# Kernel tuning notes

Hardware: AMD Instinct MI355X
Metric: run time of the kernel (lower is better)

## Reference

```python
import jax, jax.numpy as jnp
import numpy as np

N = 262144
D = 128  # hidden_dim
NUM_RULES = 5


def setup_inputs() -> dict:
    key = jax.random.key(0)
    ks = jax.random.split(key, 7)
    h_fused = jax.random.normal(ks[0], (N, D), dtype=jnp.float32)
    entity_types = jax.random.randint(ks[1], (N,), 0, 3)
    entity_masks = jnp.ones((N,), dtype=bool)
    # rule_scorer params (torch nn.Linear convention: y = x @ W.T + b)
    W1 = jax.random.normal(ks[2], (D, 3 * D), dtype=jnp.float32) * (1.0 / np.sqrt(3 * D))
    b1 = jnp.zeros((D,), dtype=jnp.float32)
    W2 = jax.random.normal(ks[3], (1, D), dtype=jnp.float32) * (1.0 / np.sqrt(D))
    b2 = jnp.zeros((1,), dtype=jnp.float32)
    rule_table = jax.random.normal(ks[4], (NUM_RULES, D), dtype=jnp.float32) * 0.1
    return {"h_fused": h_fused, "entity_types": entity_types,
            "entity_masks": entity_masks, "rule_id": 0,
            "W1": W1, "b1": b1, "W2": W2, "b2": b2, "rule_table": rule_table}


def reference(h_fused, entity_types, entity_masks, rule_id, W1, b1, W2, b2, rule_table):
    # masks per entity type
    car_mask = (entity_types == 0) & entity_masks
    light_mask = (entity_types == 1) & entity_masks
    stop_mask = (entity_types == 2) & entity_masks

    def masked_mean(mask):
        mf = mask.astype(h_fused.dtype)[:, None]            # [N,1]
        cnt = mf.sum()
        s = (h_fused * mf).sum(axis=0)                      # [D]
        return jnp.where(cnt > 0, s / jnp.maximum(cnt, 1.0), 0.0)

    h_light = masked_mean(light_mask)  # [D] - pooled once (original redundantly recomputes per car)
    h_stop = masked_mean(stop_mask)    # [D]

    n = h_fused.shape[0]
    concat = jnp.concatenate([
        h_fused,
        jnp.broadcast_to(h_light, (n, D)),
        jnp.broadcast_to(h_stop, (n, D)),
    ], axis=1)                                              # [N, 3D]

    hid = jax.nn.relu(concat @ W1.T + b1)                   # [N, D] (dropout = identity, eval)
    beta = jax.nn.sigmoid(hid @ W2.T + b2)[:, 0]            # [N]

    rule_emb = rule_table[rule_id]                          # [D]
    h_car = beta[:, None] * h_fused + (1.0 - beta[:, None]) * rule_emb
    h_out = jnp.where(car_mask[:, None], h_car, h_fused)    # [N, D]
    beta_out = jnp.where(car_mask, beta, 0.0)               # [N]; original compacts to [N_car]
    return h_out, beta_out
```

## Files before the change

kernel.cpp:

```cpp
#include <hip/hip_runtime.h>
#include <hip/hip_bf16.h>

#define D 128

typedef __attribute__((ext_vector_type(8))) short short8;
typedef __attribute__((ext_vector_type(4))) float f32x4;

__device__ __forceinline__ unsigned short f2bf(float f) {
  unsigned int u = __float_as_uint(f);
  u += 0x7FFFu + ((u >> 16) & 1u);
  return (unsigned short)(u >> 16);
}

__device__ __forceinline__ bool mask_at(const unsigned char* m, int i, bool i32layout) {
  return i32layout ? (((const int*)m)[i] != 0) : (m[i] != 0);
}


__global__ __launch_bounds__(256) void k_reduce(
    const float* __restrict__ h, const int* __restrict__ types,
    const unsigned char* __restrict__ masks, float* __restrict__ ws) {
  const int t = threadIdx.x;
  const int c4 = t & 31;
  const int rgrp = t >> 5;
  const int row0 = blockIdx.x * 256;
  const bool mi32 = (masks[1] == 0);
  __shared__ float wl_s[256], ws_s[256];
  __shared__ float redL[8][128], redS[8][128];
  {
    const int r = row0 + t;
    const int ty = types[r];
    const bool m = mask_at(masks, r, mi32);
    wl_s[t] = (ty == 1 && m) ? 1.f : 0.f;
    ws_s[t] = (ty == 2 && m) ? 1.f : 0.f;
  }
  __syncthreads();
  f32x4 sl = {0.f, 0.f, 0.f, 0.f}, ss = {0.f, 0.f, 0.f, 0.f};
  #pragma unroll 4
  for (int i = 0; i < 32; ++i) {
    const int rl = rgrp + 8 * i;
    const f32x4 v = *(const f32x4*)&h[(size_t)(row0 + rl) * D + c4 * 4];
    const float wl = wl_s[rl];
    const float w2 = ws_s[rl];
    sl += v * wl;
    ss += v * w2;
  }
  *(f32x4*)&redL[rgrp][c4 * 4] = sl;
  *(f32x4*)&redS[rgrp][c4 * 4] = ss;
  __syncthreads();
  {
    const int arr = t >> 7, col = t & 127;
    float s = 0.f;
    #pragma unroll
    for (int g = 0; g < 8; ++g) s += arr ? redS[g][col] : redL[g][col];
    atomicAdd(&ws[arr * 128 + col], s);
  }
  if (t < 64) {
    float c = wl_s[t] + wl_s[t + 64] + wl_s[t + 128] + wl_s[t + 192];
    #pragma unroll
    for (int m = 1; m < 64; m <<= 1) c += __shfl_xor(c, m, 64);
    if (t == 0) atomicAdd(&ws[256], c);
  } else if (t < 128) {
    const int u = t - 64;
    float c = ws_s[u] + ws_s[u + 64] + ws_s[u + 128] + ws_s[u + 192];
    #pragma unroll
    for (int m = 1; m < 64; m <<= 1) c += __shfl_xor(c, m, 64);
    if (t == 64) atomicAdd(&ws[257], c);
  }
}

__global__ __launch_bounds__(256) void k_prep(
    const float* __restrict__ W1, const float* __restrict__ b1,
    float* __restrict__ ws) {
  const int b = blockIdx.x;
  const int t = threadIdx.x;
  unsigned short* w1abf = (unsigned short*)(ws + 512);
  {
    const int idx = b * 256 + t;
    const int j = idx >> 7, k = idx & 127;
    w1abf[idx] = f2bf(W1[j * 384 + k]);
  }
  const int half = t >> 7, k = t & 127;
  const int j = b * 2 + half;
  const float cl = ws[256], cs = ws[257];
  const float hlk = (cl > 0.f) ? ws[k] / cl : 0.f;
  const float hsk = (cs > 0.f) ? ws[D + k] / cs : 0.f;
  float v = hlk * W1[j * 384 + 128 + k] + hsk * W1[j * 384 + 256 + k];
  #pragma unroll
  for (int m = 1; m < 64; m <<= 1) v += __shfl_xor(v, m, 64);
  __shared__ float red[4];
  if ((t & 63) == 0) red[t >> 6] = v;
  __syncthreads();
  if (t == 0) {
    ws[258 + b * 2 + 0] = red[0] + red[1] + b1[b * 2 + 0];
    ws[258 + b * 2 + 1] = red[2] + red[3] + b1[b * 2 + 1];
  }
}

__global__ __launch_bounds__(256, 2) void k_main(
    const float* __restrict__ h, const int* __restrict__ types,
    const unsigned char* __restrict__ masks,
    const int* __restrict__ rid_p,
    const float* __restrict__ W2, const float* __restrict__ b2p,
    const float* __restrict__ rule_table,
    const float* __restrict__ ws,
    float* __restrict__ out_h, float* __restrict__ out_beta) {
  __shared__ unsigned short Bs[128][136];
  __shared__ unsigned short As[64][136];
  __shared__ float cs_s[128], w2_s[128], rule_s[128];
  __shared__ float betas[64], car_s[64];

  const int t = threadIdx.x;
  const int wave = t >> 6;
  const int lane = t & 63;
  const int lrow = lane & 15;
  const int q = lane >> 4;
  const bool mi32 = (masks[1] == 0);
  const unsigned short* w1abf = (const unsigned short*)(ws + 512);
  const float* cvec = ws + 258;

  {
    const int rid = rid_p[0];
    if (t < 128) {
      cs_s[t] = cvec[t];
      rule_s[t] = rule_table[rid * D + t];
    } else {
      w2_s[t - 128] = W2[t - 128];
    }
    #pragma unroll
    for (int i = 0; i < 8; ++i) {
      const int flat = i * 256 + t;
      const int row = flat >> 4;
      const int c8 = flat & 15;
      *(uint4*)&Bs[row][c8 * 8] = *(const uint4*)&w1abf[flat * 8];
    }
  }
  __syncthreads();

  short8 breg[32];
  #pragma unroll
  for (int i = 0; i < 32; ++i) {
    const int nt = i >> 2, ks = i & 3;
    breg[i] = *(const short8*)&Bs[nt * 16 + lrow][ks * 32 + q * 8];
  }
  const float b2v = b2p[0];

  for (int tile = 0; tile < 4; ++tile) {
    const int row0 = (blockIdx.x * 4 + tile) * 64;
    #pragma unroll
    for (int i = 0; i < 8; ++i) {
      const int flat = i * 256 + t;
      const int r = flat >> 5, c4 = flat & 31;
      const f32x4 v = *(const f32x4*)&h[(size_t)(row0 + r) * D + c4 * 4];
      ushort4 bv;
      bv.x = f2bf(v.x); bv.y = f2bf(v.y); bv.z = f2bf(v.z); bv.w = f2bf(v.w);
      *(ushort4*)&As[r][c4 * 4] = bv;
    }
    __syncthreads();

    if (t < 64) {
      const int grow = row0 + t;
      car_s[t] = ((types[grow] == 0) && mask_at(masks, grow, mi32)) ? 1.f : 0.f;
    }

    short8 a[4];
    #pragma unroll
    for (int ks = 0; ks < 4; ++ks)
      a[ks] = *(const short8*)&As[wave * 16 + lrow][ks * 32 + q * 8];

    f32x4 acc[8];
    #pragma unroll
    for (int nt = 0; nt < 8; ++nt) acc[nt] = (f32x4){0.f, 0.f, 0.f, 0.f};
    #pragma unroll
    for (int nt = 0; nt < 8; ++nt) {
      #pragma unroll
      for (int ks = 0; ks < 4; ++ks)
        acc[nt] = __builtin_amdgcn_mfma_f32_16x16x32_bf16(a[ks], breg[nt * 4 + ks], acc[nt], 0, 0, 0);
    }

    float part[4] = {0.f, 0.f, 0.f, 0.f};
    #pragma unroll
    for (int nt = 0; nt < 8; ++nt) {
      const int col = nt * 16 + lrow;
      const float cv = cs_s[col];
      const float wv = w2_s[col];
      #pragma unroll
      for (int r = 0; r < 4; ++r)
        part[r] += fmaxf(acc[nt][r] + cv, 0.f) * wv;
    }
    #pragma unroll
    for (int m = 1; m < 16; m <<= 1) {
      #pragma unroll
      for (int r = 0; r < 4; ++r) part[r] += __shfl_xor(part[r], m, 64);
    }
    if (lrow == 0) {
      #pragma unroll
      for (int r = 0; r < 4; ++r) {
        const float z = part[r] + b2v;
        betas[wave * 16 + q * 4 + r] = 1.f / (1.f + __expf(-z));
      }
    }
    __syncthreads();

    #pragma unroll
    for (int i = 0; i < 4; ++i) {
      const int flat8 = i * 256 + t;
      const int r = flat8 >> 4, c8 = flat8 & 15;
      const uint4 u = *(const uint4*)&As[r][c8 * 8];
      const float beta = betas[r];
      const float cf = car_s[r];
      const float a_r = cf * beta + (1.f - cf);
      const float b_r = cf * (1.f - beta);
      f32x4 o0, o1;
      o0.x = a_r * __uint_as_float(u.x << 16)          + b_r * rule_s[c8 * 8 + 0];
      o0.y = a_r * __uint_as_float(u.x & 0xFFFF0000u)  + b_r * rule_s[c8 * 8 + 1];
      o0.z = a_r * __uint_as_float(u.y << 16)          + b_r * rule_s[c8 * 8 + 2];
      o0.w = a_r * __uint_as_float(u.y & 0xFFFF0000u)  + b_r * rule_s[c8 * 8 + 3];
      o1.x = a_r * __uint_as_float(u.z << 16)          + b_r * rule_s[c8 * 8 + 4];
      o1.y = a_r * __uint_as_float(u.z & 0xFFFF0000u)  + b_r * rule_s[c8 * 8 + 5];
      o1.z = a_r * __uint_as_float(u.w << 16)          + b_r * rule_s[c8 * 8 + 6];
      o1.w = a_r * __uint_as_float(u.w & 0xFFFF0000u)  + b_r * rule_s[c8 * 8 + 7];
      float* op = &out_h[(size_t)(row0 + r) * D + c8 * 8];
      *(f32x4*)op = o0;
      *(f32x4*)(op + 4) = o1;
    }
    if (t < 64) out_beta[row0 + t] = car_s[t] * betas[t];
    __syncthreads();
  }
}

extern "C" void kernel_launch(void* const* d_in, const int* in_sizes, int n_in,
                              void* d_out, int out_size, void* d_ws, size_t ws_size,
                              hipStream_t stream) {
  const float* h = (const float*)d_in[0];
  const int* types = (const int*)d_in[1];
  const unsigned char* masks = (const unsigned char*)d_in[2];
  const int* rid = (const int*)d_in[3];
  const float* W1 = (const float*)d_in[4];
  const float* b1 = (const float*)d_in[5];
  const float* W2 = (const float*)d_in[6];
  const float* b2 = (const float*)d_in[7];
  const float* rule_table = (const float*)d_in[8];
  float* ws = (float*)d_ws;
  const int n = in_sizes[0] / D;
  float* out_h = (float*)d_out;
  float* out_beta = out_h + (size_t)n * D;

  hipMemsetAsync(d_ws, 0, 258 * sizeof(float), stream);
  k_reduce<<<n / 256, 256, 0, stream>>>(h, types, masks, ws);
  k_prep<<<64, 256, 0, stream>>>(W1, b1, ws);
  k_main<<<n / 256, 256, 0, stream>>>(h, types, masks, rid, W2, b2, rule_table, ws,
                                      out_h, out_beta);
}
```

Before: 301.2 us.

## Double-buffer A tiles with register prefetch and stream B from LDS

The main kernel now prefetches the next 64-row tile of h into registers while the current tile's MFMA and epilogue run, then converts it into a second LDS buffer, so global load latency overlaps compute. The W1 B-fragments are read from LDS inside the MFMA loop instead of being held in 32 registers, freeing VGPRs for the prefetch. LDS row padding changes from 136 to 132, and output stores become nontemporal. The risks are more LDS traffic per tile, possible bank conflicts from the new padding, and higher register pressure from the staged values.

```diff
diff --git a/kernel.cpp b/kernel.cpp
--- a/kernel.cpp
+++ b/kernel.cpp
@@ -105,10 +105,10 @@
     const float* __restrict__ rule_table,
     const float* __restrict__ ws,
     float* __restrict__ out_h, float* __restrict__ out_beta) {
-  __shared__ unsigned short Bs[128][136];
-  __shared__ unsigned short As[64][136];
+  __shared__ unsigned short Bs[128][132];
+  __shared__ unsigned short As[2][64][132];
   __shared__ float cs_s[128], w2_s[128], rule_s[128];
-  __shared__ float betas[64], car_s[64];
+  __shared__ float betas[2][64], car_s[2][64];
 
   const int t = threadIdx.x;
   const int wave = t >> 6;
@@ -135,38 +135,51 @@
       *(uint4*)&Bs[row][c8 * 8] = *(const uint4*)&w1abf[flat * 8];
     }
   }
-  __syncthreads();
-
-  short8 breg[32];
+
+  const float b2v = b2p[0];
+  const int base = blockIdx.x * 256;
+
+  f32x4 st[8];
   #pragma unroll
-  for (int i = 0; i < 32; ++i) {
-    const int nt = i >> 2, ks = i & 3;
-    breg[i] = *(const short8*)&Bs[nt * 16 + lrow][ks * 32 + q * 8];
-  }
-  const float b2v = b2p[0];
+  for (int i = 0; i < 8; ++i) {
+    const int flat = i * 256 + t;
+    const int r = flat >> 5, c4 = flat & 31;
+    st[i] = *(const f32x4*)&h[(size_t)(base + r) * D + c4 * 4];
+  }
+  #pragma unroll
+  for (int i = 0; i < 8; ++i) {
+    const int flat = i * 256 + t;
+    const int r = flat >> 5, c4 = flat & 31;
+    ushort4 bv;
+    bv.x = f2bf(st[i].x); bv.y = f2bf(st[i].y);
+    bv.z = f2bf(st[i].z); bv.w = f2bf(st[i].w);
+    *(ushort4*)&As[0][r][c4 * 4] = bv;
+  }
+  __syncthreads();
 
   for (int tile = 0; tile < 4; ++tile) {
-    const int row0 = (blockIdx.x * 4 + tile) * 64;
-    #pragma unroll
-    for (int i = 0; i < 8; ++i) {
-      const int flat = i * 256 + t;
-      const int r = flat >> 5, c4 = flat & 31;
-      const f32x4 v = *(const f32x4*)&h[(size_t)(row0 + r) * D + c4 * 4];
-      ushort4 bv;
-      bv.x = f2bf(v.x); bv.y = f2bf(v.y); bv.z = f2bf(v.z); bv.w = f2bf(v.w);
-      *(ushort4*)&As[r][c4 * 4] = bv;
-    }
-    __syncthreads();
+    const int p = tile & 1;
+    const int row0 = base + tile * 64;
+
+    if (tile < 3) {
+      const int row0n = row0 + 64;
+      #pragma unroll
+      for (int i = 0; i < 8; ++i) {
+        const int flat = i * 256 + t;
+        const int r = flat >> 5, c4 = flat & 31;
+        st[i] = *(const f32x4*)&h[(size_t)(row0n + r) * D + c4 * 4];
+      }
+    }
 
     if (t < 64) {
       const int grow = row0 + t;
-      car_s[t] = ((types[grow] == 0) && mask_at(masks, grow, mi32)) ? 1.f : 0.f;
+      car_s[p][t] = ((types[grow] == 0) && mask_at(masks, grow, mi32)) ? 1.f : 0.f;
     }
 
     short8 a[4];
     #pragma unroll
     for (int ks = 0; ks < 4; ++ks)
-      a[ks] = *(const short8*)&As[wave * 16 + lrow][ks * 32 + q * 8];
+      a[ks] = *(const short8*)&As[p][wave * 16 + lrow][ks * 32 + q * 8];
 
     f32x4 acc[8];
     #pragma unroll
@@ -175,7 +188,9 @@
     for (int nt = 0; nt < 8; ++nt) {
       #pragma unroll
       for (int ks = 0; ks < 4; ++ks)
-        acc[nt] = __builtin_amdgcn_mfma_f32_16x16x32_bf16(a[ks], breg[nt * 4 + ks], acc[nt], 0, 0, 0);
+        acc[nt] = __builtin_amdgcn_mfma_f32_16x16x32_bf16(
+            a[ks], *(const short8*)&Bs[nt * 16 + lrow][ks * 32 + q * 8],
+            acc[nt], 0, 0, 0);
     }
 
     float part[4] = {0.f, 0.f, 0.f, 0.f};
@@ -197,7 +212,7 @@
       #pragma unroll
       for (int r = 0; r < 4; ++r) {
         const float z = part[r] + b2v;
-        betas[wave * 16 + q * 4 + r] = 1.f / (1.f + __expf(-z));
+        betas[p][wave * 16 + q * 4 + r] = 1.f / (1.f + __expf(-z));
       }
     }
     __syncthreads();
@@ -206,9 +221,9 @@
     for (int i = 0; i < 4; ++i) {
       const int flat8 = i * 256 + t;
       const int r = flat8 >> 4, c8 = flat8 & 15;
-      const uint4 u = *(const uint4*)&As[r][c8 * 8];
-      const float beta = betas[r];
-      const float cf = car_s[r];
+      const uint4 u = *(const uint4*)&As[p][r][c8 * 8];
+      const float beta = betas[p][r];
+      const float cf = car_s[p][r];
       const float a_r = cf * beta + (1.f - cf);
       const float b_r = cf * (1.f - beta);
       f32x4 o0, o1;
@@ -221,11 +236,24 @@
       o1.z = a_r * __uint_as_float(u.w << 16)          + b_r * rule_s[c8 * 8 + 6];
       o1.w = a_r * __uint_as_float(u.w & 0xFFFF0000u)  + b_r * rule_s[c8 * 8 + 7];
       float* op = &out_h[(size_t)(row0 + r) * D + c8 * 8];
-      *(f32x4*)op = o0;
-      *(f32x4*)(op + 4) = o1;
-    }
-    if (t < 64) out_beta[row0 + t] = car_s[t] * betas[t];
-    __syncthreads();
+      __builtin_nontemporal_store(o0, (f32x4*)op);
+      __builtin_nontemporal_store(o1, (f32x4*)(op + 4));
+    }
+    if (t < 64)
+      __builtin_nontemporal_store(car_s[p][t] * betas[p][t], &out_beta[row0 + t]);
+
+    if (tile < 3) {
+      #pragma unroll
+      for (int i = 0; i < 8; ++i) {
+        const int flat = i * 256 + t;
+        const int r = flat >> 5, c4 = flat & 31;
+        ushort4 bv;
+        bv.x = f2bf(st[i].x); bv.y = f2bf(st[i].y);
+        bv.z = f2bf(st[i].z); bv.w = f2bf(st[i].w);
+        *(ushort4*)&As[p ^ 1][r][c4 * 4] = bv;
+      }
+      __syncthreads();
+    }
   }
 }
 
```

Measured after the change: 302.2 us. About the same (+0.3%).

## Restructure k_main into per-wave register-prefetched tiles without A staging

Applied to the files above, without the earlier changes.

k_main now has each wave own 64 rows and load h straight into registers in MFMA fragment layout, prefetching the next 16-row tile while the current one is computed. This drops the shared-memory A tile and the block-wide barriers between tiles. The B operand is read from an XOR-swizzled shared layout on every MFMA rather than held in 32 registers, and beta is passed between lanes with shuffles. Outputs use nontemporal stores, and launch bounds move to 4 blocks per SM for more occupancy, at the cost of extra LDS reads per MFMA.

```diff
diff --git a/kernel.cpp b/kernel.cpp
--- a/kernel.cpp
+++ b/kernel.cpp
@@ -97,7 +97,7 @@
   }
 }
 
-__global__ __launch_bounds__(256, 2) void k_main(
+__global__ __launch_bounds__(256, 4) void k_main(
     const float* __restrict__ h, const int* __restrict__ types,
     const unsigned char* __restrict__ masks,
     const int* __restrict__ rid_p,
@@ -105,10 +105,8 @@
     const float* __restrict__ rule_table,
     const float* __restrict__ ws,
     float* __restrict__ out_h, float* __restrict__ out_beta) {
-  __shared__ unsigned short Bs[128][136];
-  __shared__ unsigned short As[64][136];
+  __shared__ __align__(16) unsigned short Bs[128][128];
   __shared__ float cs_s[128], w2_s[128], rule_s[128];
-  __shared__ float betas[64], car_s[64];
 
   const int t = threadIdx.x;
   const int wave = t >> 6;
@@ -118,7 +116,23 @@
   const bool mi32 = (masks[1] == 0);
   const unsigned short* w1abf = (const unsigned short*)(ws + 512);
   const float* cvec = ws + 258;
-
+  const int wbase = blockIdx.x * 256 + wave * 64;
+
+  f32x4 pf[8];
+  #pragma unroll
+  for (int ks = 0; ks < 4; ++ks) {
+    const float* src = &h[(size_t)(wbase + lrow) * D + ks * 32 + q * 8];
+    pf[ks * 2 + 0] = *(const f32x4*)src;
+    pf[ks * 2 + 1] = *(const f32x4*)(src + 4);
+  }
+
+  #pragma unroll
+  for (int i = 0; i < 8; ++i) {
+    const int flat = i * 256 + t;
+    const int row = flat >> 4;
+    const int c8 = flat & 15;
+    *(uint4*)&Bs[row][(c8 ^ (row & 7)) * 8] = *(const uint4*)&w1abf[flat * 8];
+  }
   {
     const int rid = rid_p[0];
     if (t < 128) {
@@ -127,46 +141,39 @@
     } else {
       w2_s[t - 128] = W2[t - 128];
     }
-    #pragma unroll
-    for (int i = 0; i < 8; ++i) {
-      const int flat = i * 256 + t;
-      const int row = flat >> 4;
-      const int c8 = flat & 15;
-      *(uint4*)&Bs[row][c8 * 8] = *(const uint4*)&w1abf[flat * 8];
-    }
-  }
-  __syncthreads();
-
-  short8 breg[32];
-  #pragma unroll
-  for (int i = 0; i < 32; ++i) {
-    const int nt = i >> 2, ks = i & 3;
-    breg[i] = *(const short8*)&Bs[nt * 16 + lrow][ks * 32 + q * 8];
-  }
+  }
+  __syncthreads();
+
   const float b2v = b2p[0];
 
-  for (int tile = 0; tile < 4; ++tile) {
-    const int row0 = (blockIdx.x * 4 + tile) * 64;
-    #pragma unroll
-    for (int i = 0; i < 8; ++i) {
-      const int flat = i * 256 + t;
-      const int r = flat >> 5, c4 = flat & 31;
-      const f32x4 v = *(const f32x4*)&h[(size_t)(row0 + r) * D + c4 * 4];
-      ushort4 bv;
-      bv.x = f2bf(v.x); bv.y = f2bf(v.y); bv.z = f2bf(v.z); bv.w = f2bf(v.w);
-      *(ushort4*)&As[r][c4 * 4] = bv;
-    }
-    __syncthreads();
-
-    if (t < 64) {
-      const int grow = row0 + t;
-      car_s[t] = ((types[grow] == 0) && mask_at(masks, grow, mi32)) ? 1.f : 0.f;
-    }
+  #pragma unroll
+  for (int tt = 0; tt < 4; ++tt) {
+    const int row0 = wbase + tt * 16;
+    const int myrow = row0 + lrow;
 
     short8 a[4];
     #pragma unroll
-    for (int ks = 0; ks < 4; ++ks)
-      a[ks] = *(const short8*)&As[wave * 16 + lrow][ks * 32 + q * 8];
+    for (int ks = 0; ks < 4; ++ks) {
+      const f32x4 v0 = pf[ks * 2 + 0], v1 = pf[ks * 2 + 1];
+      short8 av;
+      av[0] = (short)f2bf(v0.x); av[1] = (short)f2bf(v0.y);
+      av[2] = (short)f2bf(v0.z); av[3] = (short)f2bf(v0.w);
+      av[4] = (short)f2bf(v1.x); av[5] = (short)f2bf(v1.y);
+      av[6] = (short)f2bf(v1.z); av[7] = (short)f2bf(v1.w);
+      a[ks] = av;
+    }
+
+    if (tt < 3) {
+      const int rown = row0 + 16 + lrow;
+      #pragma unroll
+      for (int ks = 0; ks < 4; ++ks) {
+        const float* src = &h[(size_t)rown * D + ks * 32 + q * 8];
+        pf[ks * 2 + 0] = *(const f32x4*)src;
+        pf[ks * 2 + 1] = *(const f32x4*)(src + 4);
+      }
+    }
+
+    const float cf = ((types[myrow] == 0) && mask_at(masks, myrow, mi32)) ? 1.f : 0.f;
 
     f32x4 acc[8];
     #pragma unroll
@@ -175,7 +182,10 @@
     for (int nt = 0; nt < 8; ++nt) {
       #pragma unroll
       for (int ks = 0; ks < 4; ++ks)
-        acc[nt] = __builtin_amdgcn_mfma_f32_16x16x32_bf16(a[ks], breg[nt * 4 + ks], acc[nt], 0, 0, 0);
+        acc[nt] = __builtin_amdgcn_mfma_f32_16x16x32_bf16(
+            a[ks],
+            *(const short8*)&Bs[nt * 16 + lrow][((ks * 4 + q) ^ (lrow & 7)) * 8],
+            acc[nt], 0, 0, 0);
     }
 
     float part[4] = {0.f, 0.f, 0.f, 0.f};
@@ -193,39 +203,35 @@
       #pragma unroll
       for (int r = 0; r < 4; ++r) part[r] += __shfl_xor(part[r], m, 64);
     }
-    if (lrow == 0) {
-      #pragma unroll
-      for (int r = 0; r < 4; ++r) {
-        const float z = part[r] + b2v;
-        betas[wave * 16 + q * 4 + r] = 1.f / (1.f + __expf(-z));
-      }
-    }
-    __syncthreads();
-
-    #pragma unroll
-    for (int i = 0; i < 4; ++i) {
-      const int flat8 = i * 256 + t;
-      const int r = flat8 >> 4, c8 = flat8 & 15;
-      const uint4 u = *(const uint4*)&As[r][c8 * 8];
-      const float beta = betas[r];
-      const float cf = car_s[r];
-      const float a_r = cf * beta + (1.f - cf);
-      const float b_r = cf * (1.f - beta);
+    const int qs = lrow >> 2, rs = lrow & 3;
+    const int src = qs << 4;
+    const float z0 = __shfl(part[0], src, 64);
+    const float z1 = __shfl(part[1], src, 64);
+    const float z2 = __shfl(part[2], src, 64);
+    const float z3 = __shfl(part[3], src, 64);
+    const float zl = (rs & 2) ? ((rs & 1) ? z3 : z2) : ((rs & 1) ? z1 : z0);
+    const float beta = 1.f / (1.f + __expf(-(zl + b2v)));
+
+    const float a_r = cf * beta + (1.f - cf);
+    const float b_r = cf * (1.f - beta);
+    #pragma unroll
+    for (int ks = 0; ks < 4; ++ks) {
+      const int col0 = ks * 32 + q * 8;
       f32x4 o0, o1;
-      o0.x = a_r * __uint_as_float(u.x << 16)          + b_r * rule_s[c8 * 8 + 0];
-      o0.y = a_r * __uint_as_float(u.x & 0xFFFF0000u)  + b_r * rule_s[c8 * 8 + 1];
-      o0.z = a_r * __uint_as_float(u.y << 16)          + b_r * rule_s[c8 * 8 + 2];
-      o0.w = a_r * __uint_as_float(u.y & 0xFFFF0000u)  + b_r * rule_s[c8 * 8 + 3];
-      o1.x = a_r * __uint_as_float(u.z << 16)          + b_r * rule_s[c8 * 8 + 4];
-      o1.y = a_r * __uint_as_float(u.z & 0xFFFF0000u)  + b_r * rule_s[c8 * 8 + 5];
-      o1.z = a_r * __uint_as_float(u.w << 16)          + b_r * rule_s[c8 * 8 + 6];
-      o1.w = a_r * __uint_as_float(u.w & 0xFFFF0000u)  + b_r * rule_s[c8 * 8 + 7];
-      float* op = &out_h[(size_t)(row0 + r) * D + c8 * 8];
-      *(f32x4*)op = o0;
-      *(f32x4*)(op + 4) = o1;
-    }
-    if (t < 64) out_beta[row0 + t] = car_s[t] * betas[t];
-    __syncthreads();
+      o0.x = a_r * __uint_as_float(((unsigned int)(unsigned short)a[ks][0]) << 16) + b_r * rule_s[col0 + 0];
+      o0.y = a_r * __uint_as_float(((unsigned int)(unsigned short)a[ks][1]) << 16) + b_r * rule_s[col0 + 1];
+      o0.z = a_r * __uint_as_float(((unsigned int)(unsigned short)a[ks][2]) << 16) + b_r * rule_s[col0 + 2];
+      o0.w = a_r * __uint_as_float(((unsigned int)(unsigned short)a[ks][3]) << 16) + b_r * rule_s[col0 + 3];
+      o1.x = a_r * __uint_as_float(((unsigned int)(unsigned short)a[ks][4]) << 16) + b_r * rule_s[col0 + 4];
+      o1.y = a_r * __uint_as_float(((unsigned int)(unsigned short)a[ks][5]) << 16) + b_r * rule_s[col0 + 5];
+      o1.z = a_r * __uint_as_float(((unsigned int)(unsigned short)a[ks][6]) << 16) + b_r * rule_s[col0 + 6];
+      o1.w = a_r * __uint_as_float(((unsigned int)(unsigned short)a[ks][7]) << 16) + b_r * rule_s[col0 + 7];
+      float* op = &out_h[(size_t)myrow * D + col0];
+      __builtin_nontemporal_store(o0, (f32x4*)op);
+      __builtin_nontemporal_store(o1, (f32x4*)(op + 4));
+    }
+    if (lane < 16)
+      __builtin_nontemporal_store(cf * beta, &out_beta[myrow]);
   }
 }
 
```

Measured after the change: 308.8 us. 2.5% more time.
